# Kernel optimization log

Measured on AMD Instinct MI355X. Metric: run time of the kernel, lower is better.

Reference implementation:

```python
import jax, jax.numpy as jnp
import numpy as np

G, D, O, L, H, K, B = 33538, 256, 512, 6, 8, 2048, 4
FF = 4 * D
EPS = 1e-5
THRESH = 0.0


def _ln(x, s, b):
    mu = jnp.mean(x, axis=-1, keepdims=True)
    var = jnp.mean((x - mu) ** 2, axis=-1, keepdims=True)
    return (x - mu) * jax.lax.rsqrt(var + EPS) * s + b


def setup_inputs() -> dict:
    key = jax.random.key(0)
    ks = iter(jax.random.split(key, 32))
    s = 0.02
    rn = lambda shape, scale=s: jax.random.normal(next(ks), shape, dtype=jnp.float32) * scale
    inp = {
        'expr': jax.random.normal(next(ks), (B, G), dtype=jnp.float32),
        'gene_emb': rn((G, D)),
        'ep_w1': rn((D, 1), 0.5), 'ep_b1': jnp.zeros((D,), jnp.float32),
        'ep_w2': rn((D, D)), 'ep_b2': jnp.zeros((D,), jnp.float32),
        'cls': rn((D,), 1.0),
        'ln1_s': jnp.ones((L, D), jnp.float32), 'ln1_b': jnp.zeros((L, D), jnp.float32),
        'qkv_w': rn((L, 3 * D, D)), 'qkv_b': jnp.zeros((L, 3 * D), jnp.float32),
        'out_w': rn((L, D, D)), 'out_b': jnp.zeros((L, D), jnp.float32),
        'ln2_s': jnp.ones((L, D), jnp.float32), 'ln2_b': jnp.zeros((L, D), jnp.float32),
        'ff_w1': rn((L, FF, D)), 'ff_b1': jnp.zeros((L, FF), jnp.float32),
        'ff_w2': rn((L, D, FF)), 'ff_b2': jnp.zeros((L, D), jnp.float32),
        'fn_s': jnp.ones((D,), jnp.float32), 'fn_b': jnp.zeros((D,), jnp.float32),
        'pr_w1': rn((O, D)), 'pr_b1': jnp.zeros((O,), jnp.float32),
        'pr_w2': rn((O, O)), 'pr_b2': jnp.zeros((O,), jnp.float32),
    }
    return inp


def _encoder(expr, gene_emb, ep_w1, ep_b1, ep_w2, ep_b2, cls,
             ln1_s, ln1_b, qkv_w, qkv_b, out_w, out_b, ln2_s, ln2_b,
             ff_w1, ff_b1, ff_w2, ff_b2, fn_s, fn_b,
             pr_w1, pr_b1, pr_w2, pr_b2):
    Bb, Gg = expr.shape
    # --- tokeniser: token_i = gene_emb[i] + MLP(expr_i) for all genes ---
    h = jax.nn.gelu(expr[..., None] * ep_w1[:, 0] + ep_b1, approximate=False)  # [B,G,D]
    val_emb = jnp.einsum('bgd,ed->bge', h, ep_w2) + ep_b2
    tokens_all = gene_emb[None] + val_emb  # [B,G,D]
    # active-gene selection: threshold AND top-K
    active = expr > THRESH
    _, topk_idx = jax.lax.top_k(expr, K)
    sel = jnp.zeros((Bb, Gg), bool).at[jnp.arange(Bb)[:, None], topk_idx].set(True)
    active = active & sel
    counts = jnp.sum(active, axis=1)  # [B]
    # vectorized ragged packing: stable sort puts active genes (ascending id) first
    order = jnp.argsort(jnp.logical_not(active), axis=1, stable=True)[:, :K]  # [B,K]
    gathered = jnp.take_along_axis(tokens_all, order[..., None], axis=1)      # [B,K,D]
    valid = jnp.arange(K)[None, :] < counts[:, None]                          # [B,K]
    body = jnp.where(valid[..., None], gathered, 0.0)
    tokens = jnp.concatenate([jnp.broadcast_to(cls, (Bb, 1, D)), body], axis=1)  # [B,T,D]
    mask = jnp.concatenate([jnp.ones((Bb, 1), bool), valid], axis=1)             # [B,T]
    T = K + 1
    dh = D // H
    bias = jnp.where(mask, 0.0, -1e9)[:, None, None, :]  # key padding
    x = tokens
    for i in range(L):
        y = _ln(x, ln1_s[i], ln1_b[i])
        qkv = y @ qkv_w[i].T + qkv_b[i]
        q, k, v = jnp.split(qkv, 3, axis=-1)
        q = q.reshape(Bb, T, H, dh).transpose(0, 2, 1, 3)
        k = k.reshape(Bb, T, H, dh).transpose(0, 2, 1, 3)
        v = v.reshape(Bb, T, H, dh).transpose(0, 2, 1, 3)
        scores = jnp.einsum('bhqd,bhkd->bhqk', q, k) / np.sqrt(dh) + bias
        a = jax.nn.softmax(scores, axis=-1)
        o = jnp.einsum('bhqk,bhkd->bhqd', a, v).transpose(0, 2, 1, 3).reshape(Bb, T, D)
        x = x + o @ out_w[i].T + out_b[i]
        y2 = _ln(x, ln2_s[i], ln2_b[i])
        x = x + jax.nn.gelu(y2 @ ff_w1[i].T + ff_b1[i], approximate=False) @ ff_w2[i].T + ff_b2[i]
    x = _ln(x, fn_s, fn_b)
    cls_out = x[:, 0]
    return jax.nn.gelu(cls_out @ pr_w1.T + pr_b1, approximate=False) @ pr_w2.T + pr_b2


def reference(expr, gene_emb, ep_w1, ep_b1, ep_w2, ep_b2, cls,
              ln1_s, ln1_b, qkv_w, qkv_b, out_w, out_b, ln2_s, ln2_b,
              ff_w1, ff_b1, ff_w2, ff_b2, fn_s, fn_b,
              pr_w1, pr_b1, pr_w2, pr_b2):
    return _encoder(expr, gene_emb, ep_w1, ep_b1, ep_w2, ep_b2, cls,
                    ln1_s, ln1_b, qkv_w, qkv_b, out_w, out_b, ln2_s, ln2_b,
                    ff_w1, ff_b1, ff_w2, ff_b2, fn_s, fn_b,
                    pr_w1, pr_b1, pr_w2, pr_b2)
```

## Files before the change

kernel.cpp:

```cpp
#include <hip/hip_runtime.h>
#include <hip/hip_bf16.h>
#include <math.h>

#define GG 33538
#define DD 256
#define LL 6
#define HH 8
#define KK 2048
#define BB 4
#define TT 2049
#define BT (BB*TT)
#define NT 65
#define TCH 7
#define QSC (0.17677669529663688f * 1.44269504088896340f)

#if __has_builtin(__builtin_amdgcn_exp2f)
#define EXP2(x) __builtin_amdgcn_exp2f(x)
#else
#define EXP2(x) exp2f(x)
#endif

typedef __bf16 bf16x8 __attribute__((ext_vector_type(8)));
typedef float f32x4 __attribute__((ext_vector_type(4)));
typedef float f32x16 __attribute__((ext_vector_type(16)));
typedef unsigned short ub16;

union BW { __bf16 h; ub16 u; };
__device__ __forceinline__ ub16 f2b(float x) { BW w; w.h = (__bf16)x; return w.u; }
__device__ __forceinline__ unsigned pk2(float a, float b) {
    return (unsigned)f2b(a) | ((unsigned)f2b(b) << 16);
}
union U4B { unsigned u[4]; bf16x8 v; };

__device__ __forceinline__ float gelu_f(float x) {
    return 0.5f * x * (1.0f + erff(x * 0.70710678118654752440f));
}

__device__ __forceinline__ unsigned to_key(float x) {
    unsigned u = __float_as_uint(x);
    return (u & 0x80000000u) ? ~u : (u | 0x80000000u);
}

__device__ int block_scan_excl_1024(int v, int* shw) {
    int lane = threadIdx.x & 63, w = threadIdx.x >> 6;
    int x = v;
    #pragma unroll
    for (int o = 1; o < 64; o <<= 1) {
        int t = __shfl_up(x, o, 64);
        if (lane >= o) x += t;
    }
    if (lane == 63) shw[w] = x;
    __syncthreads();
    if (w == 0) {
        int y = (lane < 16) ? shw[lane] : 0;
        #pragma unroll
        for (int o = 1; o < 16; o <<= 1) {
            int t = __shfl_up(y, o, 64);
            if (lane >= o) y += t;
        }
        if (lane < 16) shw[lane] = y;
    }
    __syncthreads();
    int off = (w == 0) ? 0 : shw[w - 1];
    return off + x - v;
}

__global__ void topk_init(unsigned* __restrict__ prefwant, unsigned* __restrict__ histg) {
    int i = threadIdx.x;
    if (i < BB * 256) histg[i] = 0u;
    if (i < BB) { prefwant[2 * i] = 0u; prefwant[2 * i + 1] = KK; }
}

__global__ __launch_bounds__(1024) void topk_hist(const float* __restrict__ expr,
                                                  const unsigned* __restrict__ prefwant,
                                                  unsigned* __restrict__ histg, int pass) {
    __shared__ unsigned lh[16][256];
    int b = blockIdx.x, blk = blockIdx.y, tid = threadIdx.x, wv = tid >> 6;
    for (int i = tid; i < 16 * 256; i += 1024) ((unsigned*)lh)[i] = 0u;
    __syncthreads();
    unsigned prefix = prefwant[2 * b];
    int shift = pass * 8;
    unsigned pmask = (pass == 3) ? 0u : (0xFFFFFFFFu << (shift + 8));
    const float* row = expr + (size_t)b * GG;
    int base = blk * 5120;
    #pragma unroll
    for (int j = 0; j < 5; ++j) {
        int g = base + j * 1024 + tid;
        if (g < GG) {
            unsigned key = to_key(row[g]);
            if ((key & pmask) == (prefix & pmask))
                atomicAdd(&lh[wv][(key >> shift) & 255u], 1u);
        }
    }
    __syncthreads();
    if (tid < 256) {
        unsigned s = 0;
        #pragma unroll
        for (int j = 0; j < 16; ++j) s += lh[j][tid];
        if (s) atomicAdd(&histg[b * 256 + tid], s);
    }
}

__global__ void topk_select(unsigned* __restrict__ prefwant,
                            unsigned* __restrict__ histg, int pass) {
    int b = blockIdx.x, lane = threadIdx.x;
    int shift = pass * 8;
    unsigned pref = prefwant[2 * b];
    int want = (int)prefwant[2 * b + 1];
    unsigned cc[4];
    #pragma unroll
    for (int j = 0; j < 4; ++j) cc[j] = histg[b * 256 + lane * 4 + j];
    int s = (int)(cc[0] + cc[1] + cc[2] + cc[3]);
    int incl = s;
    #pragma unroll
    for (int o = 1; o < 64; o <<= 1) { int t = __shfl_up(incl, o); if (lane >= o) incl += t; }
    int total = __shfl(incl, 63);
    int a3 = total - incl;
    int a2 = a3 + (int)cc[3], a1 = a2 + (int)cc[2], a0 = a1 + (int)cc[1];
    int av[4] = {a0, a1, a2, a3};
    #pragma unroll
    for (int j = 0; j < 4; ++j) {
        if (av[j] < want && av[j] + (int)cc[j] >= want) {
            prefwant[2 * b] = pref | ((unsigned)(lane * 4 + j) << shift);
            prefwant[2 * b + 1] = (unsigned)(want - av[j]);
        }
    }
    #pragma unroll
    for (int j = 0; j < 4; ++j) histg[b * 256 + lane * 4 + j] = 0u;
}

__global__ __launch_bounds__(1024) void topk_c1(const float* __restrict__ expr,
                                                const unsigned* __restrict__ prefwant,
                                                int* __restrict__ blkcnt) {
    __shared__ int sred[16][2];
    int b = blockIdx.x, blk = blockIdx.y, tid = threadIdx.x;
    unsigned kth = prefwant[2 * b];
    const float* row = expr + (size_t)b * GG;
    int start = blk * 5120 + tid * 5;
    int eq = 0, gtp = 0;
    #pragma unroll
    for (int j = 0; j < 5; ++j) {
        int g = start + j;
        if (g < GG) {
            float e = row[g];
            unsigned key = to_key(e);
            eq += (key == kth);
            gtp += (key > kth && e > 0.0f);
        }
    }
    #pragma unroll
    for (int o = 1; o < 64; o <<= 1) { eq += __shfl_xor(eq, o); gtp += __shfl_xor(gtp, o); }
    if ((tid & 63) == 0) { sred[tid >> 6][0] = eq; sred[tid >> 6][1] = gtp; }
    __syncthreads();
    if (tid == 0) {
        int te = 0, tg = 0;
        #pragma unroll
        for (int i = 0; i < 16; ++i) { te += sred[i][0]; tg += sred[i][1]; }
        blkcnt[(b * TCH + blk) * 2] = te;
        blkcnt[(b * TCH + blk) * 2 + 1] = tg;
    }
}

__global__ void topk_c2(const unsigned* __restrict__ prefwant,
                        const int* __restrict__ blkcnt,
                        int* __restrict__ blkbase, int* __restrict__ cntout) {
    int b = blockIdx.x, lane = threadIdx.x;
    int eq = 0, gtp = 0;
    if (lane < TCH) {
        eq = blkcnt[(b * TCH + lane) * 2];
        gtp = blkcnt[(b * TCH + lane) * 2 + 1];
    }
    int want = (int)prefwant[2 * b + 1];
    bool kthpos = prefwant[2 * b] > 0x80000000u;
    int incl = eq;
    #pragma unroll
    for (int o = 1; o < 8; o <<= 1) { int t = __shfl_up(incl, o); if (lane >= o) incl += t; }
    int eqb = incl - eq;
    int eqsel = kthpos ? min(max(want - eqb, 0), eq) : 0;
    int act = gtp + eqsel;
    int incl2 = act;
    #pragma unroll
    for (int o = 1; o < 8; o <<= 1) { int t = __shfl_up(incl2, o); if (lane >= o) incl2 += t; }
    int outb = incl2 - act;
    if (lane < TCH) {
        blkbase[(b * TCH + lane) * 2] = eqb;
        blkbase[(b * TCH + lane) * 2 + 1] = outb;
    }
    if (lane == TCH - 1) cntout[b] = incl2;
}

__global__ __launch_bounds__(1024) void topk_c3(const float* __restrict__ expr,
                                                const unsigned* __restrict__ prefwant,
                                                const int* __restrict__ blkbase,
                                                int* __restrict__ idxout) {
    __shared__ int shw[16];
    int b = blockIdx.x, blk = blockIdx.y, tid = threadIdx.x;
    unsigned kth = prefwant[2 * b];
    int want = (int)prefwant[2 * b + 1];
    const float* row = expr + (size_t)b * GG;
    int start = blk * 5120 + tid * 5;
    int eqt = 0;
    #pragma unroll
    for (int j = 0; j < 5; ++j) {
        int g = start + j;
        if (g < GG) eqt += (to_key(row[g]) == kth);
    }
    int eqbase = blkbase[(b * TCH + blk) * 2] + block_scan_excl_1024(eqt, shw);
    __syncthreads();
    int actt = 0;
    {
        int leq = 0;
        #pragma unroll
        for (int j = 0; j < 5; ++j) {
            int g = start + j;
            if (g < GG) {
                float e = row[g];
                unsigned key = to_key(e);
                bool sel = (key > kth) || (key == kth && (eqbase + leq) < want);
                leq += (key == kth);
                actt += (sel && e > 0.0f) ? 1 : 0;
            }
        }
    }
    int pos = blkbase[(b * TCH + blk) * 2 + 1] + block_scan_excl_1024(actt, shw);
    {
        int leq = 0;
        #pragma unroll
        for (int j = 0; j < 5; ++j) {
            int g = start + j;
            if (g < GG) {
                float e = row[g];
                unsigned key = to_key(e);
                bool sel = (key > kth) || (key == kth && (eqbase + leq) < want);
                leq += (key == kth);
                if (sel && e > 0.0f) idxout[b * KK + pos++] = g;
            }
        }
    }
}

__global__ __launch_bounds__(256) void cvt_bf16_kernel(const float* __restrict__ s,
                                                       ub16* __restrict__ d, int n) {
    int i = blockIdx.x * 256 + threadIdx.x;
    if (i < n) d[i] = f2b(s[i]);
}

__global__ __launch_bounds__(256) void build_h_kernel(const float* __restrict__ expr,
                                                      const int* __restrict__ idxb,
                                                      const int* __restrict__ cntb,
                                                      const float* __restrict__ ep_w1,
                                                      const float* __restrict__ ep_b1,
                                                      ub16* __restrict__ H) {
    int i = blockIdx.x * 256 + threadIdx.x;
    int r = i >> 8, d = i & 255;
    int b = r >> 11, jj = r & (KK - 1);
    float v = 0.0f;
    if (jj < cntb[b]) {
        int g = idxb[b * KK + jj];
        float e = expr[(size_t)b * GG + g];
        v = gelu_f(e * ep_w1[d] + ep_b1[d]);
    }
    H[i] = f2b(v);
}

__global__ __launch_bounds__(256) void assemble_kernel(const float* __restrict__ VAL,
                                                       const float* __restrict__ gene_emb,
                                                       const float* __restrict__ clsv,
                                                       const int* __restrict__ idxb,
                                                       const int* __restrict__ cntb,
                                                       float* __restrict__ x) {
    int i = blockIdx.x * 256 + threadIdx.x;
    int r = i >> 8, d = i & 255;
    int b = r / TT, t = r % TT;
    float v;
    if (t == 0) {
        v = clsv[d];
    } else {
        int jj = t - 1;
        if (jj < cntb[b]) {
            int g = idxb[b * KK + jj];
            v = gene_emb[(size_t)g * DD + d] + VAL[((size_t)b * KK + jj) * DD + d];
        } else {
            v = 0.0f;
        }
    }
    x[i] = v;
}

__global__ __launch_bounds__(256) void ln_kernel(const float* __restrict__ X,
                                                 const float* __restrict__ s,
                                                 const float* __restrict__ bsh,
                                                 ub16* __restrict__ Y16,
                                                 float* __restrict__ Yf) {
    int w = threadIdx.x >> 6, lane = threadIdx.x & 63;
    size_t r = (size_t)blockIdx.x * 4 + w;
    float4 xv = *(const float4*)(X + r * 256 + lane * 4);
    float sum = xv.x + xv.y + xv.z + xv.w;
    #pragma unroll
    for (int o = 1; o < 64; o <<= 1) sum += __shfl_xor(sum, o);
    float mu = sum * (1.0f / 256.0f);
    float d0 = xv.x - mu, d1 = xv.y - mu, d2 = xv.z - mu, d3 = xv.w - mu;
    float vs = d0 * d0 + d1 * d1 + d2 * d2 + d3 * d3;
    #pragma unroll
    for (int o = 1; o < 64; o <<= 1) vs += __shfl_xor(vs, o);
    float rstd = rsqrtf(vs * (1.0f / 256.0f) + 1e-5f);
    float4 sc = *(const float4*)(s + lane * 4);
    float4 bc = *(const float4*)(bsh + lane * 4);
    float y0 = d0 * rstd * sc.x + bc.x;
    float y1 = d1 * rstd * sc.y + bc.y;
    float y2 = d2 * rstd * sc.z + bc.z;
    float y3 = d3 * rstd * sc.w + bc.w;
    if (Y16) {
        uint2 o2 = make_uint2(pk2(y0, y1), pk2(y2, y3));
        *(uint2*)(Y16 + r * 256 + lane * 4) = o2;
    } else {
        *(float4*)(Yf + r * 256 + lane * 4) = make_float4(y0, y1, y2, y3);
    }
}

__global__ __launch_bounds__(256) void gemm_bt16(const ub16* __restrict__ A,
                                                 const ub16* __restrict__ W,
                                                 const float* __restrict__ bias,
                                                 const float* __restrict__ R,
                                                 float* __restrict__ Cf,
                                                 ub16* __restrict__ Ch,
                                                 int M, int N, int K, int gelu_flag,
                                                 int qcols) {
    __shared__ ub16 As[2][64][40];
    __shared__ ub16 Ws[2][64][40];
    int tid = threadIdx.x;
    int lane = tid & 63, w = tid >> 6;
    int wr = (w >> 1) * 32, wc = (w & 1) * 32;
    int bm = blockIdx.y * 64, bn = blockIdx.x * 64;
    f32x4 acc[2][2] = {};

    int lrow = tid >> 2, lc8 = (tid & 3) * 8;
    int arow = min(bm + lrow, M - 1);
    const ub16* ap = A + (size_t)arow * K + lc8;
    const ub16* wp = W + (size_t)(bn + lrow) * K + lc8;

    int fr = lane & 15, fc = 8 * (lane >> 4);
    for (int k0 = 0; k0 < K; k0 += 64) {
        bf16x8 av0 = *(const bf16x8*)(ap + k0);
        bf16x8 av1 = *(const bf16x8*)(ap + k0 + 32);
        bf16x8 wv0 = *(const bf16x8*)(wp + k0);
        bf16x8 wv1 = *(const bf16x8*)(wp + k0 + 32);
        *(bf16x8*)&As[0][lrow][lc8] = av0;
        *(bf16x8*)&As[1][lrow][lc8] = av1;
        *(bf16x8*)&Ws[0][lrow][lc8] = wv0;
        *(bf16x8*)&Ws[1][lrow][lc8] = wv1;
        __syncthreads();
        #pragma unroll
        for (int ks = 0; ks < 2; ++ks) {
            bf16x8 a0 = *(const bf16x8*)&As[ks][wr + fr][fc];
            bf16x8 a1 = *(const bf16x8*)&As[ks][wr + 16 + fr][fc];
            bf16x8 b0 = *(const bf16x8*)&Ws[ks][wc + fr][fc];
            bf16x8 b1 = *(const bf16x8*)&Ws[ks][wc + 16 + fr][fc];
            acc[0][0] = __builtin_amdgcn_mfma_f32_16x16x32_bf16(a0, b0, acc[0][0], 0, 0, 0);
            acc[0][1] = __builtin_amdgcn_mfma_f32_16x16x32_bf16(a0, b1, acc[0][1], 0, 0, 0);
            acc[1][0] = __builtin_amdgcn_mfma_f32_16x16x32_bf16(a1, b0, acc[1][0], 0, 0, 0);
            acc[1][1] = __builtin_amdgcn_mfma_f32_16x16x32_bf16(a1, b1, acc[1][1], 0, 0, 0);
        }
        __syncthreads();
    }

    #pragma unroll
    for (int i = 0; i < 2; ++i) {
        #pragma unroll
        for (int j = 0; j < 2; ++j) {
            #pragma unroll
            for (int reg = 0; reg < 4; ++reg) {
                int gm = bm + wr + i * 16 + (lane >> 4) * 4 + reg;
                int gn = bn + wc + j * 16 + (lane & 15);
                if (gm >= M) continue;
                float v = acc[i][j][reg] + bias[gn];
                if (R) v += R[(size_t)gm * N + gn];
                if (gelu_flag) v = gelu_f(v);
                if (gn < qcols) v *= QSC;
                if (Cf) Cf[(size_t)gm * N + gn] = v;
                else    Ch[(size_t)gm * N + gn] = f2b(v);
            }
        }
    }
}

__global__ __launch_bounds__(256) void gemm_bn128(const ub16* __restrict__ A,
                                                  const ub16* __restrict__ W,
                                                  const float* __restrict__ bias,
                                                  ub16* __restrict__ Ch,
                                                  int M, int N, int K, int gelu_flag,
                                                  int qcols) {
    __shared__ ub16 As[2][64][40];
    __shared__ ub16 Ws[2][128][40];
    int tid = threadIdx.x, lane = tid & 63, w = tid >> 6;
    int wr = (w >> 1) * 32, wc = (w & 1) * 64;
    int bm = blockIdx.y * 64, bn = blockIdx.x * 128;
    f32x4 acc[2][4] = {};

    int arow = tid >> 2, aseg = tid & 3, aks = aseg >> 1, aoff = (aseg & 1) * 16;
    const ub16* apg = A + (size_t)min(bm + arow, M - 1) * K + aseg * 16;
    int wrow = tid >> 1, wks = tid & 1;
    const ub16* wpg = W + (size_t)(bn + wrow) * K + wks * 32;
    int fr = lane & 15, fc = 8 * (lane >> 4);

    bf16x8 ra0 = *(const bf16x8*)apg;
    bf16x8 ra1 = *(const bf16x8*)(apg + 8);
    bf16x8 rb0 = *(const bf16x8*)wpg;
    bf16x8 rb1 = *(const bf16x8*)(wpg + 8);
    bf16x8 rb2 = *(const bf16x8*)(wpg + 16);
    bf16x8 rb3 = *(const bf16x8*)(wpg + 24);

    for (int k0 = 0; k0 < K; k0 += 64) {
        *(bf16x8*)&As[aks][arow][aoff] = ra0;
        *(bf16x8*)&As[aks][arow][aoff + 8] = ra1;
        *(bf16x8*)&Ws[wks][wrow][0]  = rb0;
        *(bf16x8*)&Ws[wks][wrow][8]  = rb1;
        *(bf16x8*)&Ws[wks][wrow][16] = rb2;
        *(bf16x8*)&Ws[wks][wrow][24] = rb3;
        __syncthreads();
        if (k0 + 64 < K) {
            ra0 = *(const bf16x8*)(apg + k0 + 64);
            ra1 = *(const bf16x8*)(apg + k0 + 72);
            rb0 = *(const bf16x8*)(wpg + k0 + 64);
            rb1 = *(const bf16x8*)(wpg + k0 + 72);
            rb2 = *(const bf16x8*)(wpg + k0 + 80);
            rb3 = *(const bf16x8*)(wpg + k0 + 88);
        }
        #pragma unroll
        for (int ks = 0; ks < 2; ++ks) {
            bf16x8 af[2], bfv[4];
            #pragma unroll
            for (int mr = 0; mr < 2; ++mr)
                af[mr] = *(const bf16x8*)&As[ks][wr + mr * 16 + fr][fc];
            #pragma unroll
            for (int nr = 0; nr < 4; ++nr)
                bfv[nr] = *(const bf16x8*)&Ws[ks][wc + nr * 16 + fr][fc];
            #pragma unroll
            for (int mr = 0; mr < 2; ++mr)
                #pragma unroll
                for (int nr = 0; nr < 4; ++nr)
                    acc[mr][nr] = __builtin_amdgcn_mfma_f32_16x16x32_bf16(
                        af[mr], bfv[nr], acc[mr][nr], 0, 0, 0);
        }
        __syncthreads();
    }

    #pragma unroll
    for (int mr = 0; mr < 2; ++mr) {
        #pragma unroll
        for (int nr = 0; nr < 4; ++nr) {
            #pragma unroll
            for (int reg = 0; reg < 4; ++reg) {
                int gm = bm + wr + mr * 16 + (lane >> 4) * 4 + reg;
                int gn = bn + wc + nr * 16 + (lane & 15);
                if (gm >= M) continue;
                float v = acc[mr][nr][reg] + bias[gn];
                if (gelu_flag) v = gelu_f(v);
                if (gn < qcols) v *= QSC;
                Ch[(size_t)gm * N + gn] = f2b(v);
            }
        }
    }
}

__global__ __launch_bounds__(256) void kvprep(const ub16* __restrict__ qkv,
                                              ub16* __restrict__ Kc,
                                              ub16* __restrict__ Vt) {
    __shared__ unsigned vl[32][33];
    int bh = blockIdx.x, b = bh >> 3, h = bh & 7;
    int c = blockIdx.y;
    int tid = threadIdx.x;
    int krel = tid >> 2;
    int key = c * 64 + krel;
    int d8 = (tid & 3) * 8;
    U4B kv = {}, vv = {};
    if (key < TT) {
        const ub16* p = qkv + ((size_t)(b * TT + key)) * 768 + 256 + h * 32 + d8;
        kv.v = *(const bf16x8*)p;
        vv.v = *(const bf16x8*)(p + 256);
    }
    int kt = c * 2 + (krel >> 5);
    if (kt < NT)
        *(bf16x8*)(Kc + (((size_t)bh * NT + kt) * 32 + (krel & 31)) * 32 + d8) = kv.v;

    unsigned pu[4];
    #pragma unroll
    for (int j = 0; j < 4; ++j) pu[j] = __shfl_xor(vv.u[j], 4);
    if (!(krel & 1)) {
        int kp = krel >> 1;
        #pragma unroll
        for (int j = 0; j < 8; ++j) {
            unsigned mine = (vv.u[j >> 1] >> ((j & 1) * 16)) & 0xffffu;
            unsigned oth  = (pu[j >> 1] >> ((j & 1) * 16)) & 0xffffu;
            vl[d8 + j][kp] = mine | (oth << 16);
        }
    }
    __syncthreads();
    int d = tid >> 3, c8 = tid & 7;
    int kt2 = c * 2 + (c8 >> 2);
    if (kt2 < NT) {
        unsigned* vdst = (unsigned*)(Vt + (((size_t)bh * NT + kt2) * 32 + d) * 32);
        #pragma unroll
        for (int ih = 0; ih < 2; ++ih) {
            int pkr = (c8 & 3) * 4 + ih * 2;
            int dp = (pkr & 1) | ((pkr & 2) << 1) | ((pkr & 4) >> 1) | (pkr & 8);
            uint2 o2 = make_uint2(vl[d][c8 * 4 + ih * 2], vl[d][c8 * 4 + ih * 2 + 1]);
            *(uint2*)(vdst + dp) = o2;
        }
    }
}

__global__ __launch_bounds__(256) void attn_mfma7(const ub16* __restrict__ qkv,
                                                  const ub16* __restrict__ Kc,
                                                  const ub16* __restrict__ Vt,
                                                  const int* __restrict__ cnt,
                                                  ub16* __restrict__ attno) {
    __shared__ float Olds[4][32][33];
    __shared__ float Oll[4][32];
    int bh = blockIdx.x, b = bh >> 3, h = bh & 7;
    int tid = threadIdx.x;
    int w = tid >> 6, lane = tid & 63, hi = lane >> 5, q = lane & 31;
    int qt = blockIdx.y;
    int t = qt * 32 + q;
    int nvalid = cnt[b] + 1;
    int nkt = (nvalid + 31) >> 5;
    int nfull = (nvalid & 31) ? nkt - 1 : nkt;

    int tc = min(t, TT - 1);
    const ub16* qp = qkv + ((size_t)(b * TT + tc)) * 768 + h * 32 + 8 * hi;
    bf16x8 bq0 = *(const bf16x8*)qp;
    bf16x8 bq1 = *(const bf16x8*)(qp + 16);

    float l = 0.0f;
    f32x16 ot = {};

    const ub16* kbase = Kc + (size_t)bh * NT * 1024 + q * 32 + 8 * hi;
    const ub16* vbase = Vt + (size_t)bh * NT * 1024 + q * 32 + 8 * hi;

    size_t cur = (size_t)min(w, NT - 1) * 1024;
    bf16x8 ka0 = *(const bf16x8*)(kbase + cur);
    bf16x8 ka1 = *(const bf16x8*)(kbase + cur + 16);
    bf16x8 va0 = *(const bf16x8*)(vbase + cur);
    bf16x8 va1 = *(const bf16x8*)(vbase + cur + 16);

    for (int kt = w; kt < nkt; kt += 4) {
        size_t nxt = (size_t)min(kt + 4, NT - 1) * 1024;
        bf16x8 nk0 = *(const bf16x8*)(kbase + nxt);
        bf16x8 nk1 = *(const bf16x8*)(kbase + nxt + 16);
        bf16x8 nv0 = *(const bf16x8*)(vbase + nxt);
        bf16x8 nv1 = *(const bf16x8*)(vbase + nxt + 16);

        f32x16 z = {};
        f32x16 st = __builtin_amdgcn_mfma_f32_32x32x16_bf16(ka0, bq0, z, 0, 0, 0);
        st = __builtin_amdgcn_mfma_f32_32x32x16_bf16(ka1, bq1, st, 0, 0, 0);

        if (kt >= nfull) {
            int lim = nvalid - (kt << 5);
            #pragma unroll
            for (int r = 0; r < 16; ++r) {
                int off = (r & 3) + 8 * (r >> 2) + 4 * hi;
                if (off >= lim) st[r] = -1e30f;
            }
        }

        float p[16];
        #pragma unroll
        for (int r = 0; r < 16; ++r) p[r] = EXP2(st[r]);
        float s0 = (p[0] + p[1]) + (p[2] + p[3]);
        float s1 = (p[4] + p[5]) + (p[6] + p[7]);
        float s2 = (p[8] + p[9]) + (p[10] + p[11]);
        float s3 = (p[12] + p[13]) + (p[14] + p[15]);
        l += (s0 + s1) + (s2 + s3);

        bf16x8 pv0, pv1;
        #pragma unroll
        for (int jj = 0; jj < 8; ++jj) {
            pv0[jj] = (__bf16)p[jj];
            pv1[jj] = (__bf16)p[8 + jj];
        }
        ot = __builtin_amdgcn_mfma_f32_32x32x16_bf16(va0, pv0, ot, 0, 0, 0);
        ot = __builtin_amdgcn_mfma_f32_32x32x16_bf16(va1, pv1, ot, 0, 0, 0);

        ka0 = nk0; ka1 = nk1; va0 = nv0; va1 = nv1;
    }

    l += __shfl_xor(l, 32);
    #pragma unroll
    for (int r = 0; r < 16; ++r) {
        int d = (r & 3) + 8 * (r >> 2) + 4 * hi;
        Olds[w][q][d] = ot[r];
    }
    if (hi == 0) Oll[w][q] = l;
    __syncthreads();

    int qq = tid >> 3, dg = tid & 7;
    int trow = qt * 32 + qq;
    if (trow < TT) {
        float L = Oll[0][qq] + Oll[1][qq] + Oll[2][qq] + Oll[3][qq];
        float rL = 1.0f / L;
        float o[4];
        #pragma unroll
        for (int j = 0; j < 4; ++j) {
            int d = dg * 4 + j;
            o[j] = (Olds[0][qq][d] + Olds[1][qq][d] +
                    Olds[2][qq][d] + Olds[3][qq][d]) * rL;
        }
        uint2 o2 = make_uint2(pk2(o[0], o[1]), pk2(o[2], o[3]));
        *(uint2*)(attno + ((size_t)(b * TT + trow)) * 256 + h * 32 + dg * 4) = o2;
    }
}

__global__ __launch_bounds__(256) void head1_kernel(const float* __restrict__ Y,
                                                    const float* __restrict__ w1,
                                                    const float* __restrict__ b1,
                                                    float* __restrict__ t1) {
    int b = blockIdx.x, w = threadIdx.x >> 6, lane = threadIdx.x & 63;
    int o = blockIdx.y * 4 + w;
    float4 c = *(const float4*)(Y + ((size_t)b * TT) * DD + lane * 4);
    float4 ww = *(const float4*)(w1 + (size_t)o * 256 + lane * 4);
    float s = c.x * ww.x + c.y * ww.y + c.z * ww.z + c.w * ww.w;
    #pragma unroll
    for (int off = 1; off < 64; off <<= 1) s += __shfl_xor(s, off);
    if (lane == 0) t1[b * 512 + o] = gelu_f(s + b1[o]);
}

__global__ __launch_bounds__(256) void head2_kernel(const float* __restrict__ t1,
                                                    const float* __restrict__ w2,
                                                    const float* __restrict__ b2,
                                                    float* __restrict__ out) {
    int b = blockIdx.x, w = threadIdx.x >> 6, lane = threadIdx.x & 63;
    int o = blockIdx.y * 4 + w;
    const float* tp = t1 + b * 512 + lane * 8;
    const float* wp = w2 + (size_t)o * 512 + lane * 8;
    float4 a0 = *(const float4*)tp;
    float4 a1 = *(const float4*)(tp + 4);
    float4 b0 = *(const float4*)wp;
    float4 b1v = *(const float4*)(wp + 4);
    float s = a0.x * b0.x + a0.y * b0.y + a0.z * b0.z + a0.w * b0.w +
              a1.x * b1v.x + a1.y * b1v.y + a1.z * b1v.z + a1.w * b1v.w;
    #pragma unroll
    for (int off = 1; off < 64; off <<= 1) s += __shfl_xor(s, off);
    if (lane == 0) out[b * 512 + o] = s + b2[o];
}

extern "C" void kernel_launch(void* const* d_in, const int* in_sizes, int n_in,
                              void* d_out, int out_size, void* d_ws, size_t ws_size,
                              hipStream_t stream) {
    (void)in_sizes; (void)n_in; (void)out_size; (void)ws_size;
    const float* expr     = (const float*)d_in[0];
    const float* gene_emb = (const float*)d_in[1];
    const float* ep_w1    = (const float*)d_in[2];
    const float* ep_b1    = (const float*)d_in[3];
    const float* ep_w2    = (const float*)d_in[4];
    const float* ep_b2    = (const float*)d_in[5];
    const float* clsv     = (const float*)d_in[6];
    const float* ln1_s    = (const float*)d_in[7];
    const float* ln1_b    = (const float*)d_in[8];
    const float* qkv_w    = (const float*)d_in[9];
    const float* qkv_b    = (const float*)d_in[10];
    const float* out_w    = (const float*)d_in[11];
    const float* out_b    = (const float*)d_in[12];
    const float* ln2_s    = (const float*)d_in[13];
    const float* ln2_b    = (const float*)d_in[14];
    const float* ff_w1    = (const float*)d_in[15];
    const float* ff_b1    = (const float*)d_in[16];
    const float* ff_w2    = (const float*)d_in[17];
    const float* ff_b2    = (const float*)d_in[18];
    const float* fn_s     = (const float*)d_in[19];
    const float* fn_b     = (const float*)d_in[20];
    const float* pr_w1    = (const float*)d_in[21];
    const float* pr_b1    = (const float*)d_in[22];
    const float* pr_w2    = (const float*)d_in[23];
    const float* pr_b2    = (const float*)d_in[24];
    float* outp = (float*)d_out;

    const size_t KVSZ = (size_t)32 * NT * 1024;

    float* x   = (float*)d_ws;
    float* VAL = x + (size_t)BT * 256;
    ub16* y16   = (ub16*)(VAL + (size_t)8192 * 256);
    ub16* qkv16 = y16 + (size_t)BT * 256;
    ub16* att16 = qkv16 + (size_t)BT * 768;
    ub16* ff116 = att16 + (size_t)BT * 256;
    ub16* kc_h  = ff116 + (size_t)BT * 1024;
    ub16* wqkv  = kc_h + KVSZ;
    ub16* wout  = wqkv + (size_t)LL * 768 * 256;
    ub16* wff1  = wout + (size_t)LL * 256 * 256;
    ub16* wff2  = wff1 + (size_t)LL * 1024 * 256;
    ub16* wep2  = wff2 + (size_t)LL * 256 * 1024;
    int*  idxb  = (int*)(wep2 + (size_t)256 * 256);
    int*  cntb  = idxb + BB * KK;
    unsigned* prefwant = (unsigned*)(cntb + BB);
    unsigned* histg    = prefwant + BB * 2;
    int* blkcnt  = (int*)(histg + BB * 256);
    int* blkbase = blkcnt + BB * TCH * 2;
    float* t1f   = (float*)(blkbase + BB * TCH * 2);
    ub16* H16 = kc_h;
    ub16* Kc  = kc_h;
    ub16* Vt  = (ub16*)VAL;

    topk_init<<<1, 1024, 0, stream>>>(prefwant, histg);
    for (int p = 3; p >= 0; --p) {
        topk_hist<<<dim3(BB, TCH), 1024, 0, stream>>>(expr, prefwant, histg, p);
        topk_select<<<BB, 64, 0, stream>>>(prefwant, histg, p);
    }
    topk_c1<<<dim3(BB, TCH), 1024, 0, stream>>>(expr, prefwant, blkcnt);
    topk_c2<<<BB, 64, 0, stream>>>(prefwant, blkcnt, blkbase, cntb);
    topk_c3<<<dim3(BB, TCH), 1024, 0, stream>>>(expr, prefwant, blkbase, idxb);

    cvt_bf16_kernel<<<(LL*768*256 + 255)/256, 256, 0, stream>>>(qkv_w, wqkv, LL*768*256);
    cvt_bf16_kernel<<<(LL*256*256 + 255)/256, 256, 0, stream>>>(out_w, wout, LL*256*256);
    cvt_bf16_kernel<<<(LL*1024*256 + 255)/256, 256, 0, stream>>>(ff_w1, wff1, LL*1024*256);
    cvt_bf16_kernel<<<(LL*256*1024 + 255)/256, 256, 0, stream>>>(ff_w2, wff2, LL*256*1024);
    cvt_bf16_kernel<<<(256*256 + 255)/256, 256, 0, stream>>>(ep_w2, wep2, 256*256);

    build_h_kernel<<<(BB * KK * DD) / 256, 256, 0, stream>>>(expr, idxb, cntb, ep_w1, ep_b1, H16);
    gemm_bt16<<<dim3(4, 128), 256, 0, stream>>>(H16, wep2, ep_b2, nullptr, VAL, nullptr,
                                                8192, 256, 256, 0, 0);
    assemble_kernel<<<BT, 256, 0, stream>>>(VAL, gene_emb, clsv, idxb, cntb, x);

    for (int i = 0; i < LL; ++i) {
        ln_kernel<<<BT / 4, 256, 0, stream>>>(x, ln1_s + i * DD, ln1_b + i * DD, y16, nullptr);
        gemm_bn128<<<dim3(6, 129), 256, 0, stream>>>(y16, wqkv + (size_t)i * 768 * 256,
                                                     qkv_b + i * 768, qkv16,
                                                     BT, 768, 256, 0, 256);
        kvprep<<<dim3(BB * HH, 33), 256, 0, stream>>>(qkv16, Kc, Vt);
        attn_mfma7<<<dim3(BB * HH, NT), 256, 0, stream>>>(qkv16, Kc, Vt, cntb, att16);
        gemm_bt16<<<dim3(4, 129), 256, 0, stream>>>(att16, wout + (size_t)i * 256 * 256,
                                                    out_b + i * 256, x, x, nullptr,
                                                    BT, 256, 256, 0, 0);
        ln_kernel<<<BT / 4, 256, 0, stream>>>(x, ln2_s + i * DD, ln2_b + i * DD, y16, nullptr);
        gemm_bn128<<<dim3(8, 129), 256, 0, stream>>>(y16, wff1 + (size_t)i * 1024 * 256,
                                                     ff_b1 + i * 1024, ff116,
                                                     BT, 1024, 256, 1, 0);
        gemm_bt16<<<dim3(4, 129), 256, 0, stream>>>(ff116, wff2 + (size_t)i * 256 * 1024,
                                                    ff_b2 + i * 256, x, x, nullptr,
                                                    BT, 256, 1024, 0, 0);
    }

    ln_kernel<<<BT / 4, 256, 0, stream>>>(x, fn_s, fn_b, nullptr, VAL);
    head1_kernel<<<dim3(BB, 128), 256, 0, stream>>>(VAL, pr_w1, pr_b1, t1f);
    head2_kernel<<<dim3(BB, 128), 256, 0, stream>>>(t1f, pr_w2, pr_b2, outp);
}
```

Before: 825.2 us.

## Software-pipeline QK scores in attention and unify GEMMs on 64x128 tile kernel

The attention loop now computes the QK^T scores for the next key tile before the softmax and PV step of the current one, and prefetches K two tiles ahead. This lets the score MFMAs overlap the exp and convert work, at the cost of more registers. Separately, the 64x64 gemm_bt16 kernel is removed. gemm_bn128 gains residual add and fp32 output so it can handle the N=256 projections as well. That halves the block count for those GEMMs (2x129), which raises per-block reuse but lowers parallelism.

```diff
diff --git a/kernel.cpp b/kernel.cpp
--- a/kernel.cpp
+++ b/kernel.cpp
@@ -318,75 +318,11 @@
     }
 }
 
-__global__ __launch_bounds__(256) void gemm_bt16(const ub16* __restrict__ A,
-                                                 const ub16* __restrict__ W,
-                                                 const float* __restrict__ bias,
-                                                 const float* __restrict__ R,
-                                                 float* __restrict__ Cf,
-                                                 ub16* __restrict__ Ch,
-                                                 int M, int N, int K, int gelu_flag,
-                                                 int qcols) {
-    __shared__ ub16 As[2][64][40];
-    __shared__ ub16 Ws[2][64][40];
-    int tid = threadIdx.x;
-    int lane = tid & 63, w = tid >> 6;
-    int wr = (w >> 1) * 32, wc = (w & 1) * 32;
-    int bm = blockIdx.y * 64, bn = blockIdx.x * 64;
-    f32x4 acc[2][2] = {};
-
-    int lrow = tid >> 2, lc8 = (tid & 3) * 8;
-    int arow = min(bm + lrow, M - 1);
-    const ub16* ap = A + (size_t)arow * K + lc8;
-    const ub16* wp = W + (size_t)(bn + lrow) * K + lc8;
-
-    int fr = lane & 15, fc = 8 * (lane >> 4);
-    for (int k0 = 0; k0 < K; k0 += 64) {
-        bf16x8 av0 = *(const bf16x8*)(ap + k0);
-        bf16x8 av1 = *(const bf16x8*)(ap + k0 + 32);
-        bf16x8 wv0 = *(const bf16x8*)(wp + k0);
-        bf16x8 wv1 = *(const bf16x8*)(wp + k0 + 32);
-        *(bf16x8*)&As[0][lrow][lc8] = av0;
-        *(bf16x8*)&As[1][lrow][lc8] = av1;
-        *(bf16x8*)&Ws[0][lrow][lc8] = wv0;
-        *(bf16x8*)&Ws[1][lrow][lc8] = wv1;
-        __syncthreads();
-        #pragma unroll
-        for (int ks = 0; ks < 2; ++ks) {
-            bf16x8 a0 = *(const bf16x8*)&As[ks][wr + fr][fc];
-            bf16x8 a1 = *(const bf16x8*)&As[ks][wr + 16 + fr][fc];
-            bf16x8 b0 = *(const bf16x8*)&Ws[ks][wc + fr][fc];
-            bf16x8 b1 = *(const bf16x8*)&Ws[ks][wc + 16 + fr][fc];
-            acc[0][0] = __builtin_amdgcn_mfma_f32_16x16x32_bf16(a0, b0, acc[0][0], 0, 0, 0);
-            acc[0][1] = __builtin_amdgcn_mfma_f32_16x16x32_bf16(a0, b1, acc[0][1], 0, 0, 0);
-            acc[1][0] = __builtin_amdgcn_mfma_f32_16x16x32_bf16(a1, b0, acc[1][0], 0, 0, 0);
-            acc[1][1] = __builtin_amdgcn_mfma_f32_16x16x32_bf16(a1, b1, acc[1][1], 0, 0, 0);
-        }
-        __syncthreads();
-    }
-
-    #pragma unroll
-    for (int i = 0; i < 2; ++i) {
-        #pragma unroll
-        for (int j = 0; j < 2; ++j) {
-            #pragma unroll
-            for (int reg = 0; reg < 4; ++reg) {
-                int gm = bm + wr + i * 16 + (lane >> 4) * 4 + reg;
-                int gn = bn + wc + j * 16 + (lane & 15);
-                if (gm >= M) continue;
-                float v = acc[i][j][reg] + bias[gn];
-                if (R) v += R[(size_t)gm * N + gn];
-                if (gelu_flag) v = gelu_f(v);
-                if (gn < qcols) v *= QSC;
-                if (Cf) Cf[(size_t)gm * N + gn] = v;
-                else    Ch[(size_t)gm * N + gn] = f2b(v);
-            }
-        }
-    }
-}
-
 __global__ __launch_bounds__(256) void gemm_bn128(const ub16* __restrict__ A,
                                                   const ub16* __restrict__ W,
                                                   const float* __restrict__ bias,
+                                                  const float* __restrict__ R,
+                                                  float* __restrict__ Cf,
                                                   ub16* __restrict__ Ch,
                                                   int M, int N, int K, int gelu_flag,
                                                   int qcols) {
@@ -455,9 +391,11 @@
                 int gn = bn + wc + nr * 16 + (lane & 15);
                 if (gm >= M) continue;
                 float v = acc[mr][nr][reg] + bias[gn];
+                if (R) v += R[(size_t)gm * N + gn];
                 if (gelu_flag) v = gelu_f(v);
                 if (gn < qcols) v *= QSC;
-                Ch[(size_t)gm * N + gn] = f2b(v);
+                if (Cf) Cf[(size_t)gm * N + gn] = v;
+                else    Ch[(size_t)gm * N + gn] = f2b(v);
             }
         }
     }
@@ -510,7 +448,7 @@
     }
 }
 
-__global__ __launch_bounds__(256) void attn_mfma7(const ub16* __restrict__ qkv,
+__global__ __launch_bounds__(256) void attn_mfma8(const ub16* __restrict__ qkv,
                                                   const ub16* __restrict__ Kc,
                                                   const ub16* __restrict__ Vt,
                                                   const int* __restrict__ cnt,
@@ -537,51 +475,65 @@
     const ub16* kbase = Kc + (size_t)bh * NT * 1024 + q * 32 + 8 * hi;
     const ub16* vbase = Vt + (size_t)bh * NT * 1024 + q * 32 + 8 * hi;
 
-    size_t cur = (size_t)min(w, NT - 1) * 1024;
-    bf16x8 ka0 = *(const bf16x8*)(kbase + cur);
-    bf16x8 ka1 = *(const bf16x8*)(kbase + cur + 16);
-    bf16x8 va0 = *(const bf16x8*)(vbase + cur);
-    bf16x8 va1 = *(const bf16x8*)(vbase + cur + 16);
+    size_t o0 = (size_t)min(w, NT - 1) * 1024;
+    size_t o1 = (size_t)min(w + 4, NT - 1) * 1024;
+    bf16x8 ka0 = *(const bf16x8*)(kbase + o0);
+    bf16x8 ka1 = *(const bf16x8*)(kbase + o0 + 16);
+    bf16x8 va0 = *(const bf16x8*)(vbase + o0);
+    bf16x8 va1 = *(const bf16x8*)(vbase + o0 + 16);
+    bf16x8 kb0 = *(const bf16x8*)(kbase + o1);
+    bf16x8 kb1 = *(const bf16x8*)(kbase + o1 + 16);
+
+    f32x16 z = {};
+    f32x16 st = __builtin_amdgcn_mfma_f32_32x32x16_bf16(ka0, bq0, z, 0, 0, 0);
+    st = __builtin_amdgcn_mfma_f32_32x32x16_bf16(ka1, bq1, st, 0, 0, 0);
+    if (w >= nfull) {
+        int lim = nvalid - (w << 5);
+        #pragma unroll
+        for (int r = 0; r < 16; ++r) {
+            int off = (r & 3) + 8 * (r >> 2) + 4 * hi;
+            if (off >= lim) st[r] = -1e30f;
+        }
+    }
 
     for (int kt = w; kt < nkt; kt += 4) {
-        size_t nxt = (size_t)min(kt + 4, NT - 1) * 1024;
-        bf16x8 nk0 = *(const bf16x8*)(kbase + nxt);
-        bf16x8 nk1 = *(const bf16x8*)(kbase + nxt + 16);
-        bf16x8 nv0 = *(const bf16x8*)(vbase + nxt);
-        bf16x8 nv1 = *(const bf16x8*)(vbase + nxt + 16);
-
-        f32x16 z = {};
-        f32x16 st = __builtin_amdgcn_mfma_f32_32x32x16_bf16(ka0, bq0, z, 0, 0, 0);
-        st = __builtin_amdgcn_mfma_f32_32x32x16_bf16(ka1, bq1, st, 0, 0, 0);
-
-        if (kt >= nfull) {
-            int lim = nvalid - (kt << 5);
+        size_t o2 = (size_t)min(kt + 8, NT - 1) * 1024;
+        size_t ov = (size_t)min(kt + 4, NT - 1) * 1024;
+        bf16x8 kc0 = *(const bf16x8*)(kbase + o2);
+        bf16x8 kc1 = *(const bf16x8*)(kbase + o2 + 16);
+        bf16x8 vb0 = *(const bf16x8*)(vbase + ov);
+        bf16x8 vb1 = *(const bf16x8*)(vbase + ov + 16);
+
+        f32x16 stn = __builtin_amdgcn_mfma_f32_32x32x16_bf16(kb0, bq0, z, 0, 0, 0);
+        stn = __builtin_amdgcn_mfma_f32_32x32x16_bf16(kb1, bq1, stn, 0, 0, 0);
+        if (kt + 4 >= nfull) {
+            int lim = nvalid - ((kt + 4) << 5);
             #pragma unroll
             for (int r = 0; r < 16; ++r) {
                 int off = (r & 3) + 8 * (r >> 2) + 4 * hi;
-                if (off >= lim) st[r] = -1e30f;
+                if (off >= lim) stn[r] = -1e30f;
             }
         }
 
-        float p[16];
-        #pragma unroll
-        for (int r = 0; r < 16; ++r) p[r] = EXP2(st[r]);
-        float s0 = (p[0] + p[1]) + (p[2] + p[3]);
-        float s1 = (p[4] + p[5]) + (p[6] + p[7]);
-        float s2 = (p[8] + p[9]) + (p[10] + p[11]);
-        float s3 = (p[12] + p[13]) + (p[14] + p[15]);
+        #pragma unroll
+        for (int r = 0; r < 16; ++r) st[r] = EXP2(st[r]);
+        float s0 = (st[0] + st[1]) + (st[2] + st[3]);
+        float s1 = (st[4] + st[5]) + (st[6] + st[7]);
+        float s2 = (st[8] + st[9]) + (st[10] + st[11]);
+        float s3 = (st[12] + st[13]) + (st[14] + st[15]);
         l += (s0 + s1) + (s2 + s3);
 
         bf16x8 pv0, pv1;
         #pragma unroll
         for (int jj = 0; jj < 8; ++jj) {
-            pv0[jj] = (__bf16)p[jj];
-            pv1[jj] = (__bf16)p[8 + jj];
+            pv0[jj] = (__bf16)st[jj];
+            pv1[jj] = (__bf16)st[8 + jj];
         }
         ot = __builtin_amdgcn_mfma_f32_32x32x16_bf16(va0, pv0, ot, 0, 0, 0);
         ot = __builtin_amdgcn_mfma_f32_32x32x16_bf16(va1, pv1, ot, 0, 0, 0);
 
-        ka0 = nk0; ka1 = nk1; va0 = nv0; va1 = nv1;
+        st = stn;
+        kb0 = kc0; kb1 = kc1; va0 = vb0; va1 = vb1;
     }
 
     l += __shfl_xor(l, 32);
@@ -715,27 +667,27 @@
     cvt_bf16_kernel<<<(256*256 + 255)/256, 256, 0, stream>>>(ep_w2, wep2, 256*256);
 
     build_h_kernel<<<(BB * KK * DD) / 256, 256, 0, stream>>>(expr, idxb, cntb, ep_w1, ep_b1, H16);
-    gemm_bt16<<<dim3(4, 128), 256, 0, stream>>>(H16, wep2, ep_b2, nullptr, VAL, nullptr,
-                                                8192, 256, 256, 0, 0);
+    gemm_bn128<<<dim3(2, 128), 256, 0, stream>>>(H16, wep2, ep_b2, nullptr, VAL, nullptr,
+                                                 8192, 256, 256, 0, 0);
     assemble_kernel<<<BT, 256, 0, stream>>>(VAL, gene_emb, clsv, idxb, cntb, x);
 
     for (int i = 0; i < LL; ++i) {
         ln_kernel<<<BT / 4, 256, 0, stream>>>(x, ln1_s + i * DD, ln1_b + i * DD, y16, nullptr);
         gemm_bn128<<<dim3(6, 129), 256, 0, stream>>>(y16, wqkv + (size_t)i * 768 * 256,
-                                                     qkv_b + i * 768, qkv16,
+                                                     qkv_b + i * 768, nullptr, nullptr, qkv16,
                                                      BT, 768, 256, 0, 256);
         kvprep<<<dim3(BB * HH, 33), 256, 0, stream>>>(qkv16, Kc, Vt);
-        attn_mfma7<<<dim3(BB * HH, NT), 256, 0, stream>>>(qkv16, Kc, Vt, cntb, att16);
-        gemm_bt16<<<dim3(4, 129), 256, 0, stream>>>(att16, wout + (size_t)i * 256 * 256,
-                                                    out_b + i * 256, x, x, nullptr,
-                                                    BT, 256, 256, 0, 0);
+        attn_mfma8<<<dim3(BB * HH, NT), 256, 0, stream>>>(qkv16, Kc, Vt, cntb, att16);
+        gemm_bn128<<<dim3(2, 129), 256, 0, stream>>>(att16, wout + (size_t)i * 256 * 256,
+                                                     out_b + i * 256, x, x, nullptr,
+                                                     BT, 256, 256, 0, 0);
         ln_kernel<<<BT / 4, 256, 0, stream>>>(x, ln2_s + i * DD, ln2_b + i * DD, y16, nullptr);
         gemm_bn128<<<dim3(8, 129), 256, 0, stream>>>(y16, wff1 + (size_t)i * 1024 * 256,
-                                                     ff_b1 + i * 1024, ff116,
+                                                     ff_b1 + i * 1024, nullptr, nullptr, ff116,
                                                      BT, 1024, 256, 1, 0);
-        gemm_bt16<<<dim3(4, 129), 256, 0, stream>>>(ff116, wff2 + (size_t)i * 256 * 1024,
-                                                    ff_b2 + i * 256, x, x, nullptr,
-                                                    BT, 256, 1024, 0, 0);
+        gemm_bn128<<<dim3(2, 129), 256, 0, stream>>>(ff116, wff2 + (size_t)i * 256 * 1024,
+                                                     ff_b2 + i * 256, x, x, nullptr,
+                                                     BT, 256, 1024, 0, 0);
     }
 
     ln_kernel<<<BT / 4, 256, 0, stream>>>(x, fn_s, fn_b, nullptr, VAL);
```

Measured after the change: 907.4 us. 1.1x slower.
